# Kernel tuning notes

Hardware: AMD Instinct MI355X
Metric: run time of the kernel (lower is better)

The kernel has to match this reference:

```python
import jax, jax.numpy as jnp
import numpy as np

B, S, HID = 1, 4096, 2048
NH, NKV, HD = 16, 4, 128
BLK, LOCAL, GLOB, STRIDE = 128, 4, 4, 8
NEG = -1e9


def _rotate_half(x):
    x1 = x[..., : x.shape[-1] // 2]
    x2 = x[..., x.shape[-1] // 2 :]
    return jnp.concatenate([-x2, x1], axis=-1)


def setup_inputs() -> dict:
    key = jax.random.key(0)
    ks = jax.random.split(key, 6)
    hidden_states = jax.random.normal(ks[0], (B, S, HID), jnp.float32)
    attention_mask_2d = jnp.ones((B, S), jnp.float32)
    # RoPE tables (b=1 broadcasts over batch, heads)
    pos = jnp.arange(S, dtype=jnp.float32)
    inv = 1.0 / (10000.0 ** (jnp.arange(0, HD, 2, dtype=jnp.float32) / HD))
    fr = pos[:, None] * inv[None, :]
    emb = jnp.concatenate([fr, fr], axis=-1)
    cos = jnp.cos(emb)[None]
    sin = jnp.sin(emb)[None]
    sc = 0.02
    Wq = jax.random.normal(ks[1], (HID, NH * HD), jnp.float32) * sc
    Wk = jax.random.normal(ks[2], (HID, NKV * HD), jnp.float32) * sc
    Wv = jax.random.normal(ks[3], (HID, NKV * HD), jnp.float32) * sc
    Wo = jax.random.normal(ks[4], (NH * HD, HID), jnp.float32) * sc
    return dict(hidden_states=hidden_states, attention_mask_2d=attention_mask_2d,
                cos=cos, sin=sin, Wq=Wq, Wk=Wk, Wv=Wv, Wo=Wo)


def reference(hidden_states, attention_mask_2d, cos, sin, Wq, Wk, Wv, Wo):
    b, Sq, _ = hidden_states.shape
    q = (hidden_states @ Wq).reshape(b, Sq, NH, HD).transpose(0, 2, 1, 3)
    k = (hidden_states @ Wk).reshape(b, Sq, NKV, HD).transpose(0, 2, 1, 3)
    v = (hidden_states @ Wv).reshape(b, Sq, NKV, HD).transpose(0, 2, 1, 3)
    c, s = cos[:, None], sin[:, None]  # broadcast over heads
    q = q * c + _rotate_half(q) * s
    k = k * c + _rotate_half(k) * s
    rep = NH // NKV
    k = jnp.repeat(k, rep, axis=1)
    v = jnp.repeat(v, rep, axis=1)

    scaling = HD ** -0.5
    N = Sq // BLK  # seq divisible by block_size -> pad=0 in the original
    qb = q.reshape(b, NH, N, BLK, HD).astype(jnp.float32)
    kb = k.reshape(b, NH, N, BLK, HD).astype(jnp.float32)
    vb = v.reshape(b, NH, N, BLK, HD).astype(jnp.float32)
    km = attention_mask_2d.reshape(b, N, BLK)

    # ---- local windows: LOCAL blocks ending at the current block ----
    Lp = LOCAL - 1
    kp = jnp.pad(kb, ((0, 0), (0, 0), (Lp, 0), (0, 0), (0, 0)))
    vp = jnp.pad(vb, ((0, 0), (0, 0), (Lp, 0), (0, 0), (0, 0)))
    kmp = jnp.pad(km, ((0, 0), (Lp, 0), (0, 0)))  # padded blocks masked (0)
    win = jnp.arange(N)[:, None] + jnp.arange(LOCAL)[None, :]  # (N, LOCAL)
    k_local = kp[:, :, win]          # (b,h,N,LOCAL,BLK,HD)
    v_local = vp[:, :, win]
    km_local = kmp[:, win]           # (b,N,LOCAL,BLK)

    s_local = jnp.einsum('bhntd,bhnlsd->bhntls', qb, k_local) * scaling
    s_local = s_local + (1.0 - km_local)[:, None, :, None, :, :] * NEG
    intra = jnp.triu(jnp.full((BLK, BLK), NEG, jnp.float32), 1)  # causal inside current block only
    s_local = s_local.at[:, :, :, :, -1, :].add(intra)
    s_local = s_local.reshape(b, NH, N, BLK, LOCAL * BLK)

    # ---- global blocks: block 0 + strided past blocks, dedup -> masked ----
    i = jnp.arange(N)
    offsets = jnp.arange(GLOB - 1, 0, -1) * STRIDE
    idx = jnp.clip(i[:, None] - offsets[None, :], 0)
    idx = jnp.concatenate([jnp.zeros((N, 1), idx.dtype), idx], axis=1)  # (N, GLOB)
    dup = idx[:, 1:] == idx[:, :-1]
    g_valid = jnp.concatenate([jnp.ones((N, 1), bool), ~dup], axis=1).astype(jnp.float32)
    k_g = kb[:, :, idx]              # (b,h,N,GLOB,BLK,HD) gather of global blocks
    v_g = vb[:, :, idx]
    km_g = km[:, idx] * g_valid[None, :, :, None]  # (b,N,GLOB,BLK)

    s_g = jnp.einsum('bhntd,bhngsd->bhntgs', qb, k_g) * scaling
    s_g = s_g + (1.0 - km_g)[:, None, :, None, :, :] * NEG
    s_g = s_g.reshape(b, NH, N, BLK, GLOB * BLK)

    scores = jnp.concatenate([s_local, s_g], axis=-1)  # (b,h,N,BLK,(LOCAL+GLOB)*BLK)
    v_all = jnp.concatenate([v_local.reshape(b, NH, N, LOCAL * BLK, HD),
                             v_g.reshape(b, NH, N, GLOB * BLK, HD)], axis=-2)
    probs = jax.nn.softmax(scores, axis=-1)  # dropout_p = 0 (eval)
    out = jnp.einsum('bhntk,bhnkd->bhntd', probs, v_all)
    out = out.reshape(b, NH, Sq, HD).transpose(0, 2, 1, 3).reshape(b, Sq, NH * HD)
    return out @ Wo
```

## Files before the change

### kernel.cpp

```cpp
#include <hip/hip_runtime.h>
#include <hip/hip_bf16.h>
#include <cstdint>

#define NEGV   (-1000000000.0f)
#define SCALE  0.08838834764831845f
#define LOG2E  1.4426950408889634f
#define QSC    (SCALE * LOG2E)
#define NEGL2  (NEGV * LOG2E)

typedef __bf16 bf16x8 __attribute__((ext_vector_type(8)));
typedef float  f32x4  __attribute__((ext_vector_type(4)));
typedef unsigned short u16;
typedef unsigned int   u32;

#define MFMA16(a, b, c) __builtin_amdgcn_mfma_f32_16x16x32_bf16((a), (b), (c), 0, 0, 0)

#define WS_XP    ((size_t)0)
#define WS_AOP   ((size_t)0)
#define WS_WQP   ((size_t)8388608)
#define WS_WKP   ((size_t)12582912)
#define WS_WVP   ((size_t)13631488)
#define WS_WOP   ((size_t)14680064)
#define WS_QF    ((size_t)18874368)
#define WS_KF    ((size_t)27262976)
#define WS_VF    ((size_t)29360128)

__device__ __forceinline__ u16 f2bf(float f) {
  union { float f; u32 u; } v; v.f = f;
  u32 u = v.u;
  u += 0x7FFFu + ((u >> 16) & 1u);
  return (u16)(u >> 16);
}

__device__ __forceinline__ void gl_lds16(const u16* g, u16* l) {
  __builtin_amdgcn_global_load_lds((const __attribute__((address_space(1))) u32*)g,
                                   (__attribute__((address_space(3))) u32*)l,
                                   16, 0, 0);
}

__device__ __forceinline__ int fragoff(int row, int k) {
  return ((row >> 4) * 64 + ((k >> 3) & 3) * 16 + (row & 15)) * 8 + (k & 7);
}

__global__ __launch_bounds__(256, 4)
void convert_kernel(const float* __restrict__ X,
                    const float* __restrict__ Wq,
                    const float* __restrict__ Wk,
                    const float* __restrict__ Wv,
                    const float* __restrict__ Wo,
                    u16* __restrict__ ws)
{
  const int t = blockIdx.x;
  const int tid = threadIdx.x;
  const float* src; u16* dst; int tt, ldn; bool amode = false;
  if (t < 2048)      { src = X;  dst = ws + WS_XP;  tt = t;        ldn = 2048; amode = true; }
  else if (t < 3072) { src = Wq; dst = ws + WS_WQP; tt = t - 2048; ldn = 2048; }
  else if (t < 3328) { src = Wk; dst = ws + WS_WKP; tt = t - 3072; ldn = 512;  }
  else if (t < 3584) { src = Wv; dst = ws + WS_WVP; tt = t - 3328; ldn = 512;  }
  else               { src = Wo; dst = ws + WS_WOP; tt = t - 3584; ldn = 2048; }
  const int rb = tt >> 6, kb = tt & 63;

  if (amode) {
    #pragma unroll
    for (int p = 0; p < 2; ++p) {
      const int c = tid + 256 * p;
      const int row = (c >> 6) * 16 + (c & 15);
      const int k0  = ((c >> 4) & 3) * 8;
      union { u16 h[8]; uint4 v; } pk;
      const float* s0 = src + (size_t)(rb * 128 + row) * 2048 + kb * 32 + k0;
      const float4 a0 = *reinterpret_cast<const float4*>(s0);
      const float4 a1 = *reinterpret_cast<const float4*>(s0 + 4);
      pk.h[0] = f2bf(a0.x); pk.h[1] = f2bf(a0.y); pk.h[2] = f2bf(a0.z); pk.h[3] = f2bf(a0.w);
      pk.h[4] = f2bf(a1.x); pk.h[5] = f2bf(a1.y); pk.h[6] = f2bf(a1.z); pk.h[7] = f2bf(a1.w);
      *reinterpret_cast<uint4*>(dst + (size_t)tt * 4096 + c * 8) = pk.v;
    }
  } else {
    __shared__ u16 Ls[32][136];
    #pragma unroll
    for (int i = 0; i < 4; ++i) {
      const int c = tid + 256 * i;
      const int k = c >> 5, n4 = c & 31;
      const float4 wv = *reinterpret_cast<const float4*>(
          src + (size_t)(kb * 32 + k) * ldn + rb * 128 + n4 * 4);
      u16* d = &Ls[k][n4 * 4];
      d[0] = f2bf(wv.x); d[1] = f2bf(wv.y); d[2] = f2bf(wv.z); d[3] = f2bf(wv.w);
    }
    __syncthreads();
    #pragma unroll
    for (int p = 0; p < 2; ++p) {
      const int c = tid + 256 * p;
      const int row = (c >> 6) * 16 + (c & 15);
      const int k0  = ((c >> 4) & 3) * 8;
      union { u16 h[8]; uint4 v; } pk;
      #pragma unroll
      for (int j = 0; j < 8; ++j) pk.h[j] = Ls[k0 + j][row];
      *reinterpret_cast<uint4*>(dst + (size_t)tt * 4096 + c * 8) = pk.v;
    }
  }
}

__device__ __forceinline__ void gemm_core(const u16* __restrict__ pa,
                                          const u16* __restrict__ pb,
                                          u16* As, u16* Bs,
                                          int tid, int wave, int lane,
                                          f32x4 acc[2][8])
{
  for (int it = 0; it < 64; ++it) {
    __syncthreads();
    gl_lds16(pa + tid * 8,         As + tid * 8);
    gl_lds16(pa + (tid + 256) * 8, As + (tid + 256) * 8);
    gl_lds16(pb + tid * 8,         Bs + tid * 8);
    gl_lds16(pb + (tid + 256) * 8, Bs + (tid + 256) * 8);
    pa += 4096; pb += 4096;
    __syncthreads();
    bf16x8 af0 = *reinterpret_cast<const bf16x8*>(As + (wave * 2 + 0) * 512 + lane * 8);
    bf16x8 af1 = *reinterpret_cast<const bf16x8*>(As + (wave * 2 + 1) * 512 + lane * 8);
    #pragma unroll
    for (int nt = 0; nt < 8; ++nt) {
      const bf16x8 bfr = *reinterpret_cast<const bf16x8*>(Bs + nt * 512 + lane * 8);
      acc[0][nt] = MFMA16(af0, bfr, acc[0][nt]);
      acc[1][nt] = MFMA16(af1, bfr, acc[1][nt]);
    }
  }
}

__global__ __launch_bounds__(256, 3)
void qkv_kernel(const float* __restrict__ cosp,
                const float* __restrict__ sinp,
                u16* __restrict__ ws)
{
  const int mb = blockIdx.x, bn = blockIdx.y;
  const int tid = threadIdx.x;
  const int wave = tid >> 6, lane = tid & 63;
  const int lq = lane >> 4, l16 = lane & 15;

  const u16* Ab = ws + WS_XP + (size_t)mb * 64 * 4096;
  const u16* Bb; int seg, hh;
  if (bn < 16)      { Bb = ws + WS_WQP + (size_t)bn * 64 * 4096;        seg = 0; hh = bn; }
  else if (bn < 20) { Bb = ws + WS_WKP + (size_t)(bn - 16) * 64 * 4096; seg = 1; hh = bn - 16; }
  else              { Bb = ws + WS_WVP + (size_t)(bn - 20) * 64 * 4096; seg = 2; hh = bn - 20; }

  __shared__ __align__(16) u16 As[4096];
  __shared__ __align__(16) u16 Bs[4096];

  f32x4 acc[2][8];
  #pragma unroll
  for (int i = 0; i < 2; ++i)
    #pragma unroll
    for (int j = 0; j < 8; ++j)
      #pragma unroll
      for (int r = 0; r < 4; ++r) acc[i][j][r] = 0.0f;

  gemm_core(Ab, Bb, As, Bs, tid, wave, lane, acc);

  const int m0 = mb * 128;
  if (seg == 2) {
    u16* V = ws + WS_VF + (size_t)hh * 524288;
    #pragma unroll
    for (int mt = 0; mt < 2; ++mt)
      #pragma unroll
      for (int nt = 0; nt < 8; ++nt) {
        const int d = nt * 16 + l16;
        #pragma unroll
        for (int r = 0; r < 4; ++r) {
          const int s = m0 + wave * 32 + mt * 16 + lq * 4 + r;
          V[(s >> 5) * 4096 + fragoff(d, s & 31)] = f2bf(acc[mt][nt][r]);
        }
      }
  } else {
    u16* D = ws + ((seg == 0) ? WS_QF : WS_KF) + (size_t)hh * 524288;
    const float qs = (seg == 0) ? QSC : 1.0f;
    #pragma unroll
    for (int mt = 0; mt < 2; ++mt)
      #pragma unroll
      for (int r = 0; r < 4; ++r) {
        const int s = m0 + wave * 32 + mt * 16 + lq * 4 + r;
        const int sl = s & 127;
        u16* Dt = D + (size_t)(s >> 7) * 16384;
        #pragma unroll
        for (int nt = 0; nt < 4; ++nt) {
          const int d1 = nt * 16 + l16, d2 = d1 + 64;
          const float c  = cosp[s * 128 + d1];
          const float sn = sinp[s * 128 + d1];
          const float v1 = acc[mt][nt][r], v2 = acc[mt][nt + 4][r];
          Dt[(d1 >> 5) * 4096 + fragoff(sl, d1 & 31)] = f2bf((v1 * c - v2 * sn) * qs);
          Dt[(d2 >> 5) * 4096 + fragoff(sl, d2 & 31)] = f2bf((v2 * c + v1 * sn) * qs);
        }
      }
  }
}

__global__ __launch_bounds__(512, 4)
void attn_kernel(const float* __restrict__ amask, u16* __restrict__ ws)
{
  const int n = blockIdx.x, h = blockIdx.y;
  const int kvh = h >> 2;
  const int tid = threadIdx.x;
  const int wave = tid >> 6, lane = tid & 63;
  const int lq = lane >> 4, l16 = lane & 15;

  const u16* Kfb = ws + WS_KF + (size_t)kvh * 524288;
  const u16* Vfb = ws + WS_VF + (size_t)kvh * 524288;
  u16* AOp = ws + WS_AOP;

  __shared__ __align__(16) u16 bufK[16384];
  __shared__ __align__(16) u16 bufV[16384];

  const u16* Qb = ws + WS_QF + (size_t)h * 524288 + (size_t)n * 16384;
  bf16x8 qf[4];
  #pragma unroll
  for (int kk = 0; kk < 4; ++kk)
    qf[kk] = *reinterpret_cast<const bf16x8*>(Qb + (size_t)kk * 4096 + (wave * 64 + lane) * 8);

  f32x4 O[8];
  #pragma unroll
  for (int j = 0; j < 8; ++j)
    #pragma unroll
    for (int r = 0; r < 4; ++r) O[j][r] = 0.0f;
  float mrow[4], lrow[4];
  #pragma unroll
  for (int r = 0; r < 4; ++r) { mrow[r] = -3.0e38f; lrow[r] = 0.0f; }

  int gidx[4]; bool gval[4];
  gidx[0] = 0;
  gidx[1] = (n - 24 > 0) ? n - 24 : 0;
  gidx[2] = (n - 16 > 0) ? n - 16 : 0;
  gidx[3] = (n - 8  > 0) ? n - 8  : 0;
  gval[0] = true;
  gval[1] = (gidx[1] != gidx[0]);
  gval[2] = (gidx[2] != gidx[1]);
  gval[3] = (gidx[3] != gidx[2]);

  for (int kb = 0; kb < 8; ++kb) {
    int bkey; bool bvalid; bool intra;
    if (kb < 4) { bkey = n - 3 + kb; bvalid = (bkey >= 0); intra = (kb == 3); }
    else        { bkey = gidx[kb - 4]; bvalid = gval[kb - 4]; intra = false; }
    if (!bvalid) continue;

    const u16* Kb = Kfb + (size_t)bkey * 16384;
    const u16* Vb = Vfb + (size_t)bkey * 16384;
    __syncthreads();
    #pragma unroll
    for (int p = 0; p < 4; ++p) {
      gl_lds16(Kb + (tid + 512 * p) * 8, bufK + (tid + 512 * p) * 8);
      gl_lds16(Vb + (tid + 512 * p) * 8, bufV + (tid + 512 * p) * 8);
    }
    __syncthreads();

    f32x4 sacc[8];
    #pragma unroll
    for (int j = 0; j < 8; ++j)
      #pragma unroll
      for (int r = 0; r < 4; ++r) sacc[j][r] = 0.0f;
    #pragma unroll
    for (int kk = 0; kk < 4; ++kk)
      #pragma unroll
      for (int nt = 0; nt < 8; ++nt) {
        const bf16x8 bfr = *reinterpret_cast<const bf16x8*>(
            bufK + ((kk * 8 + nt) * 64 + lane) * 8);
        sacc[nt] = MFMA16(qf[kk], bfr, sacc[nt]);
      }

    float bias[8];
    #pragma unroll
    for (int nt = 0; nt < 8; ++nt)
      bias[nt] = (1.0f - amask[bkey * 128 + nt * 16 + l16]) * NEGL2;

    __syncthreads();

    u16* pw = bufK + wave * 2048;
    #pragma unroll
    for (int r = 0; r < 4; ++r) {
      const int tq = wave * 16 + lq * 4 + r;
      float sv[8];
      float rmax = -3.0e38f;
      #pragma unroll
      for (int nt = 0; nt < 8; ++nt) {
        float s = sacc[nt][r] + bias[nt];
        const int tk = nt * 16 + l16;
        if (intra && tk > tq) s += NEGL2;
        sv[nt] = s;
        rmax = fmaxf(rmax, s);
      }
      #pragma unroll
      for (int off = 1; off < 16; off <<= 1)
        rmax = fmaxf(rmax, __shfl_xor(rmax, off, 64));
      const float mold = mrow[r];
      const float mnew = fmaxf(mold, rmax);
      const float alpha = exp2f(mold - mnew);
      float rsum = 0.0f;
      u16 pb[8];
      #pragma unroll
      for (int nt = 0; nt < 8; ++nt) {
        const float pe = exp2f(sv[nt] - mnew);
        rsum += pe;
        pb[nt] = f2bf(pe);
      }
      #pragma unroll
      for (int off = 1; off < 16; off <<= 1)
        rsum += __shfl_xor(rsum, off, 64);
      lrow[r] = lrow[r] * alpha + rsum;
      mrow[r] = mnew;
      #pragma unroll
      for (int nt = 0; nt < 8; ++nt) O[nt][r] *= alpha;
      #pragma unroll
      for (int nt = 0; nt < 8; ++nt)
        pw[(nt >> 1) * 512 + ((((nt & 1) * 2 + (l16 >> 3)) * 16) + lq * 4 + r) * 8 + (l16 & 7)] = pb[nt];
    }

    #pragma unroll
    for (int kk = 0; kk < 4; ++kk) {
      const bf16x8 pf = *reinterpret_cast<const bf16x8*>(pw + kk * 512 + lane * 8);
      #pragma unroll
      for (int nt = 0; nt < 8; ++nt) {
        const bf16x8 vfr = *reinterpret_cast<const bf16x8*>(
            bufV + ((kk * 8 + nt) * 64 + lane) * 8);
        O[nt] = MFMA16(pf, vfr, O[nt]);
      }
    }
  }

  #pragma unroll
  for (int r = 0; r < 4; ++r) {
    const float inv = 1.0f / lrow[r];
    const int s = n * 128 + wave * 16 + lq * 4 + r;
    #pragma unroll
    for (int nt = 0; nt < 8; ++nt) {
      const int kcol = h * 128 + nt * 16 + l16;
      AOp[((size_t)(s >> 7) * 64 + (kcol >> 5)) * 4096 + fragoff(s & 127, kcol & 31)] =
          f2bf(O[nt][r] * inv);
    }
  }
}

__global__ __launch_bounds__(256, 3)
void outproj_kernel(const u16* __restrict__ ws, float* __restrict__ Out)
{
  const int mb = blockIdx.x, bn = blockIdx.y;
  const int tid = threadIdx.x;
  const int wave = tid >> 6, lane = tid & 63;
  const int lq = lane >> 4, l16 = lane & 15;

  const u16* Ab = ws + WS_AOP + (size_t)mb * 64 * 4096;
  const u16* Bb = ws + WS_WOP + (size_t)bn * 64 * 4096;

  __shared__ __align__(16) u16 As[4096];
  __shared__ __align__(16) u16 Bs[4096];

  f32x4 acc[2][8];
  #pragma unroll
  for (int i = 0; i < 2; ++i)
    #pragma unroll
    for (int j = 0; j < 8; ++j)
      #pragma unroll
      for (int r = 0; r < 4; ++r) acc[i][j][r] = 0.0f;

  gemm_core(Ab, Bb, (u16*)As, (u16*)Bs, tid, wave, lane, acc);

  #pragma unroll
  for (int mt = 0; mt < 2; ++mt)
    #pragma unroll
    for (int nt = 0; nt < 8; ++nt) {
      const int ccol = bn * 128 + nt * 16 + l16;
      #pragma unroll
      for (int r = 0; r < 4; ++r) {
        const int s = mb * 128 + wave * 32 + mt * 16 + lq * 4 + r;
        Out[(size_t)s * 2048 + ccol] = acc[mt][nt][r];
      }
    }
}

extern "C" void kernel_launch(void* const* d_in, const int* in_sizes, int n_in,
                              void* d_out, int out_size, void* d_ws, size_t ws_size,
                              hipStream_t stream) {
  const float* X     = (const float*)d_in[0];
  const float* amask = (const float*)d_in[1];
  const float* cosp  = (const float*)d_in[2];
  const float* sinp  = (const float*)d_in[3];
  const float* Wq    = (const float*)d_in[4];
  const float* Wk    = (const float*)d_in[5];
  const float* Wv    = (const float*)d_in[6];
  const float* Wo    = (const float*)d_in[7];
  float* Out = (float*)d_out;
  u16* ws = (u16*)d_ws;

  hipLaunchKernelGGL(convert_kernel, dim3(4608), dim3(256), 0, stream,
                     X, Wq, Wk, Wv, Wo, ws);
  hipLaunchKernelGGL(qkv_kernel, dim3(32, 24), dim3(256), 0, stream,
                     cosp, sinp, ws);
  hipLaunchKernelGGL(attn_kernel, dim3(32, 16), dim3(512), 0, stream,
                     amask, ws);
  hipLaunchKernelGGL(outproj_kernel, dim3(32, 16), dim3(256), 0, stream,
                     ws, Out);
}
```

Measured before the change: 298.8 us.

## Restructure attention block loop: precomputed bias, dedicated P buffer, reversed block order

The attention kernel now computes the list of valid key blocks up front instead of skipping invalid ones inside the loop. It stages the mask bias for all those blocks in shared memory once per workgroup. P tiles go to a separate per-wave shared buffer in small chunks rather than reusing the K buffer, which removes one __syncthreads per key block. Block index order is reversed so the heaviest query blocks launch first. The cost is dynamic shared memory (about 76 KB per workgroup), which may lower occupancy, plus a hipFuncSetAttribute call on every launch.

```diff
diff --git a/kernel.cpp b/kernel.cpp
--- a/kernel.cpp
+++ b/kernel.cpp
@@ -193,7 +193,14 @@
 __global__ __launch_bounds__(512, 4)
 void attn_kernel(const float* __restrict__ amask, u16* __restrict__ ws)
 {
-  const int n = blockIdx.x, h = blockIdx.y;
+  extern __shared__ __align__(16) u16 smem[];
+  u16* bufK = smem;
+  u16* bufV = smem + 16384;
+  u16* Pch  = smem + 32768;
+  float* biasL = (float*)(smem + 36864);
+
+  const int n = 31 - blockIdx.x;
+  const int h = blockIdx.y;
   const int kvh = h >> 2;
   const int tid = threadIdx.x;
   const int wave = tid >> 6, lane = tid & 63;
@@ -202,9 +209,7 @@
   const u16* Kfb = ws + WS_KF + (size_t)kvh * 524288;
   const u16* Vfb = ws + WS_VF + (size_t)kvh * 524288;
   u16* AOp = ws + WS_AOP;
-
-  __shared__ __align__(16) u16 bufK[16384];
-  __shared__ __align__(16) u16 bufV[16384];
+  u16* Pw = Pch + wave * 512;
 
   const u16* Qb = ws + WS_QF + (size_t)h * 524288 + (size_t)n * 16384;
   bf16x8 qf[4];
@@ -221,24 +226,29 @@
   #pragma unroll
   for (int r = 0; r < 4; ++r) { mrow[r] = -3.0e38f; lrow[r] = 0.0f; }
 
-  int gidx[4]; bool gval[4];
-  gidx[0] = 0;
-  gidx[1] = (n - 24 > 0) ? n - 24 : 0;
-  gidx[2] = (n - 16 > 0) ? n - 16 : 0;
-  gidx[3] = (n - 8  > 0) ? n - 8  : 0;
-  gval[0] = true;
-  gval[1] = (gidx[1] != gidx[0]);
-  gval[2] = (gidx[2] != gidx[1]);
-  gval[3] = (gidx[3] != gidx[2]);
-
-  for (int kb = 0; kb < 8; ++kb) {
-    int bkey; bool bvalid; bool intra;
-    if (kb < 4) { bkey = n - 3 + kb; bvalid = (bkey >= 0); intra = (kb == 3); }
-    else        { bkey = gidx[kb - 4]; bvalid = gval[kb - 4]; intra = false; }
-    if (!bvalid) continue;
-
+  const int L = (n < 3 ? n : 3) + 1;
+  const int G = (n >= 25) ? 3 : (n >= 17) ? 2 : (n >= 9) ? 1 : 0;
+  const int nv = L + 1 + G;
+  #define KBOF(i) ((i) < L ? n - L + 1 + (i) : ((i) == L ? 0 : n - 8 * (G - ((i) - L - 1))))
+
+  {
+    const int t = tid & 127;
+    #pragma unroll
+    for (int p = 0; p < 2; ++p) {
+      const int i = (tid >> 7) + p * 4;
+      if (i < nv) {
+        const int b = KBOF(i);
+        biasL[i * 128 + t] = (1.0f - amask[b * 128 + t]) * NEGL2;
+      }
+    }
+  }
+
+  for (int i = 0; i < nv; ++i) {
+    const int bkey = KBOF(i);
+    const bool intra = (i == L - 1);
     const u16* Kb = Kfb + (size_t)bkey * 16384;
     const u16* Vb = Vfb + (size_t)bkey * 16384;
+
     __syncthreads();
     #pragma unroll
     for (int p = 0; p < 4; ++p) {
@@ -264,11 +274,9 @@
     float bias[8];
     #pragma unroll
     for (int nt = 0; nt < 8; ++nt)
-      bias[nt] = (1.0f - amask[bkey * 128 + nt * 16 + l16]) * NEGL2;
-
-    __syncthreads();
-
-    u16* pw = bufK + wave * 2048;
+      bias[nt] = biasL[i * 128 + nt * 16 + l16];
+
+    u32 pbp[4][4];
     #pragma unroll
     for (int r = 0; r < 4; ++r) {
       const int tq = wave * 16 + lq * 4 + r;
@@ -289,12 +297,12 @@
       const float mnew = fmaxf(mold, rmax);
       const float alpha = exp2f(mold - mnew);
       float rsum = 0.0f;
-      u16 pb[8];
       #pragma unroll
       for (int nt = 0; nt < 8; ++nt) {
         const float pe = exp2f(sv[nt] - mnew);
         rsum += pe;
-        pb[nt] = f2bf(pe);
+        if (nt & 1) pbp[r][nt >> 1] |= (u32)f2bf(pe) << 16;
+        else        pbp[r][nt >> 1]  = (u32)f2bf(pe);
       }
       #pragma unroll
       for (int off = 1; off < 16; off <<= 1)
@@ -303,22 +311,26 @@
       mrow[r] = mnew;
       #pragma unroll
       for (int nt = 0; nt < 8; ++nt) O[nt][r] *= alpha;
-      #pragma unroll
-      for (int nt = 0; nt < 8; ++nt)
-        pw[(nt >> 1) * 512 + ((((nt & 1) * 2 + (l16 >> 3)) * 16) + lq * 4 + r) * 8 + (l16 & 7)] = pb[nt];
-    }
-
-    #pragma unroll
-    for (int kk = 0; kk < 4; ++kk) {
-      const bf16x8 pf = *reinterpret_cast<const bf16x8*>(pw + kk * 512 + lane * 8);
+    }
+
+    #pragma unroll
+    for (int c = 0; c < 4; ++c) {
+      #pragma unroll
+      for (int r = 0; r < 4; ++r) {
+        const u32 pk2 = pbp[r][c];
+        Pw[(((l16 >> 3)) * 16 + lq * 4 + r) * 8 + (l16 & 7)]     = (u16)pk2;
+        Pw[((2 + (l16 >> 3)) * 16 + lq * 4 + r) * 8 + (l16 & 7)] = (u16)(pk2 >> 16);
+      }
+      const bf16x8 pf = *reinterpret_cast<const bf16x8*>(Pw + lane * 8);
       #pragma unroll
       for (int nt = 0; nt < 8; ++nt) {
         const bf16x8 vfr = *reinterpret_cast<const bf16x8*>(
-            bufV + ((kk * 8 + nt) * 64 + lane) * 8);
+            bufV + ((c * 8 + nt) * 64 + lane) * 8);
         O[nt] = MFMA16(pf, vfr, O[nt]);
       }
     }
   }
+  #undef KBOF
 
   #pragma unroll
   for (int r = 0; r < 4; ++r) {
@@ -384,11 +396,14 @@
   float* Out = (float*)d_out;
   u16* ws = (u16*)d_ws;
 
+  (void)hipFuncSetAttribute((const void*)attn_kernel,
+                            hipFuncAttributeMaxDynamicSharedMemorySize, 77824);
+
   hipLaunchKernelGGL(convert_kernel, dim3(4608), dim3(256), 0, stream,
                      X, Wq, Wk, Wv, Wo, ws);
   hipLaunchKernelGGL(qkv_kernel, dim3(32, 24), dim3(256), 0, stream,
                      cosp, sinp, ws);
-  hipLaunchKernelGGL(attn_kernel, dim3(32, 16), dim3(512), 0, stream,
+  hipLaunchKernelGGL(attn_kernel, dim3(32, 16), dim3(512), 77824, stream,
                      amask, ws);
   hipLaunchKernelGGL(outproj_kernel, dim3(32, 16), dim3(256), 0, stream,
                      ws, Out);
```

After: 286.1 us. -4.3%, faster.
